# Performance work log

Hardware: AMD Instinct MI355X
Metric: run time of the kernel (lower is better)

## Reference

```python
import jax, jax.numpy as jnp
import numpy as np

# Photon library / detector geometry constants
NX, NY, NZ = 64, 64, 64          # voxel grid
N_VOX = NX * NY * NZ             # 262,144 voxels
N_PMT = 180                      # number of PMTs (columns of vis LUT)
N_CLUSTERS = 128                 # number of charge clusters (= len(dx))
PTS_PER_CLUSTER = 8192
TOTAL = N_CLUSTERS * PTS_PER_CLUSTER  # 1,048,576 charge points
LOWER = jnp.array([0.0, 0.0, 0.0], dtype=jnp.float32)
VOXEL_SIZE = jnp.array([1.0, 1.0, 1.0], dtype=jnp.float32)


def coord_to_voxel(coords):
    """Uniform-grid voxelization; x is the fastest-varying index so that
    vox_id + 1 is the neighbor voxel along x (matches the original backward)."""
    idx = jnp.floor((coords - LOWER) / VOXEL_SIZE).astype(jnp.int32)
    idx = jnp.clip(idx, 0, jnp.array([NX - 1, NY - 1, NZ - 1], dtype=jnp.int32))
    return idx[:, 0] + NX * (idx[:, 1] + NY * idx[:, 2])


def setup_inputs() -> dict:
    key = jax.random.key(0)
    k1, k2, k3, k4 = jax.random.split(key, 4)
    # coords: x in [8, 56) so dx in [-5, 5] stays in-grid; y,z in [0, 64)
    xyz = jax.random.uniform(
        k1, (TOTAL, 3),
        minval=jnp.array([8.0, 0.0, 0.0]),
        maxval=jnp.array([56.0, 64.0, 64.0]),
        dtype=jnp.float32,
    )
    q = jax.random.uniform(k2, (TOTAL, 1), dtype=jnp.float32)  # charge > 0
    batch = jnp.concatenate([xyz, q], axis=1)  # [TOTAL, 4]
    sizes = jnp.full((N_CLUSTERS,), PTS_PER_CLUSTER, dtype=jnp.int32)
    dx = jax.random.uniform(k3, (N_CLUSTERS,), minval=-3.0, maxval=3.0,
                            dtype=jnp.float32)
    dx_ranges = jnp.stack(
        [jnp.full((N_CLUSTERS,), -5.0, dtype=jnp.float32),
         jnp.full((N_CLUSTERS,), 5.0, dtype=jnp.float32)], axis=1)
    vis = jax.random.uniform(k4, (N_VOX, N_PMT), dtype=jnp.float32) * 1e-3
    return {"dx": dx, "batch": batch, "sizes": sizes,
            "dx_ranges": dx_ranges, "vis": vis}


def reference(dx, batch, sizes, dx_ranges, vis):
    # mask_dx(clamp=True): clamp per-cluster offsets to their ranges
    dx_c = jnp.clip(dx, dx_ranges[:, 0], dx_ranges[:, 1])  # [N_CLUSTERS]
    # cluster id per point (torch.repeat_interleave / torch.split equivalent)
    seg = jnp.repeat(jnp.arange(N_CLUSTERS, dtype=jnp.int32), sizes,
                     total_repeat_length=TOTAL)  # [TOTAL]
    coords = batch[:, :3].at[:, 0].add(dx_c[seg])  # shift x per cluster
    q = batch[:, 3]
    vox_ids = coord_to_voxel(coords)               # [TOTAL] int32
    vis_q = vis[vox_ids] * q[:, None]              # [TOTAL, N_PMT] gather+scale
    # ragged per-cluster sum (torch.split + per-segment sum, fused)
    pred = jax.ops.segment_sum(vis_q, seg, num_segments=N_CLUSTERS)
    return pred  # [N_CLUSTERS, N_PMT]
```

## Files before the change

### kernel.cpp

```cpp
#include <hip/hip_runtime.h>

#define N_PMT 180
#define N_PMT4 45
#define N_CLUSTERS 128
#define BPC 16
#define BLOCK 256
#define NWAVE (BLOCK / 64)


__global__ void prep_kernel(const float* __restrict__ dx,
                            const int* __restrict__ sizes,
                            const float* __restrict__ dx_ranges,
                            int* __restrict__ offsets,
                            float* __restrict__ dxc) {
    __shared__ int s[N_CLUSTERS];
    const int t = threadIdx.x;
    s[t] = sizes[t];
    float lo = dx_ranges[2 * t];
    float hi = dx_ranges[2 * t + 1];
    dxc[t] = fminf(fmaxf(dx[t], lo), hi);
    __syncthreads();
    int acc = 0;
    for (int i = 0; i < t; ++i) acc += s[i];
    offsets[t] = acc;
    if (t == N_CLUSTERS - 1) offsets[N_CLUSTERS] = acc + s[t];
}

__global__ __launch_bounds__(BLOCK) void gather_kernel(
    const float4* __restrict__ batch,
    const float4* __restrict__ vis4,
    const int*    __restrict__ offsets,
    const float*  __restrict__ dxc,
    float* __restrict__ out) {

    const int b     = blockIdx.x;
    const int c     = b / BPC;
    const int sub   = b % BPC;
    const int start = offsets[c];
    const int end   = offsets[c + 1];
    const int count = end - start;
    const int chunk = (count + BPC - 1) / BPC;
    const int s0 = start + sub * chunk;
    const int s1 = min(s0 + chunk, end);

    const int wave = threadIdx.x >> 6;
    const int lane = threadIdx.x & 63;

    const int wtotal = s1 - s0;
    const int per = (wtotal + NWAVE - 1) / NWAVE;
    const int ws0 = s0 + wave * per;
    const int ws1 = min(ws0 + per, s1);

    const float dxc_c = dxc[c];
    const bool active = (lane < N_PMT4);

    float4 accE = {0.f, 0.f, 0.f, 0.f};
    float4 accO = {0.f, 0.f, 0.f, 0.f};

    for (int base = ws0; base < ws1; base += 64) {
        const int p = base + lane;
        float q = 0.f;
        int vox = 0;
        if (p < ws1) {
            float4 pd = batch[p];
            float x = pd.x + dxc_c;
            int ix = (int)floorf(x);
            int iy = (int)floorf(pd.y);
            int iz = (int)floorf(pd.z);
            ix = max(0, min(63, ix));
            iy = max(0, min(63, iy));
            iz = max(0, min(63, iz));
            vox = ix + 64 * (iy + 64 * iz);
            q = pd.w;
        }
        #pragma unroll
        for (int j = 0; j < 64; j += 2) {
            const int   v0 = __builtin_amdgcn_readlane(vox, j);
            const float q0 = __uint_as_float(__builtin_amdgcn_readlane(__float_as_uint(q), j));
            const int   v1 = __builtin_amdgcn_readlane(vox, j + 1);
            const float q1 = __uint_as_float(__builtin_amdgcn_readlane(__float_as_uint(q), j + 1));
            if (active) {
                float4 r0 = vis4[(size_t)v0 * N_PMT4 + lane];
                float4 r1 = vis4[(size_t)v1 * N_PMT4 + lane];
                accE.x = fmaf(r0.x, q0, accE.x);
                accE.y = fmaf(r0.y, q0, accE.y);
                accE.z = fmaf(r0.z, q0, accE.z);
                accE.w = fmaf(r0.w, q0, accE.w);
                accO.x = fmaf(r1.x, q1, accO.x);
                accO.y = fmaf(r1.y, q1, accO.y);
                accO.z = fmaf(r1.z, q1, accO.z);
                accO.w = fmaf(r1.w, q1, accO.w);
            }
        }
    }

    __shared__ float sacc[N_PMT];
    for (int i = threadIdx.x; i < N_PMT; i += BLOCK) sacc[i] = 0.f;
    __syncthreads();
    if (active) {
        atomicAdd(&sacc[lane * 4 + 0], accE.x + accO.x);
        atomicAdd(&sacc[lane * 4 + 1], accE.y + accO.y);
        atomicAdd(&sacc[lane * 4 + 2], accE.z + accO.z);
        atomicAdd(&sacc[lane * 4 + 3], accE.w + accO.w);
    }
    __syncthreads();
    for (int i = threadIdx.x; i < N_PMT; i += BLOCK)
        atomicAdd(&out[c * N_PMT + i], sacc[i]);
}

extern "C" void kernel_launch(void* const* d_in, const int* in_sizes, int n_in,
                              void* d_out, int out_size, void* d_ws, size_t ws_size,
                              hipStream_t stream) {
    const float* dx        = (const float*)d_in[0];
    const float* batch     = (const float*)d_in[1];
    const int*   sizes     = (const int*)d_in[2];
    const float* dx_ranges = (const float*)d_in[3];
    const float* vis       = (const float*)d_in[4];
    float* out = (float*)d_out;

    int*   offsets = (int*)d_ws;
    float* dxc     = (float*)((char*)d_ws + sizeof(int) * (N_CLUSTERS + 1));

    hipMemsetAsync(out, 0, (size_t)out_size * sizeof(float), stream);

    prep_kernel<<<1, N_CLUSTERS, 0, stream>>>(dx, sizes, dx_ranges, offsets, dxc);

    gather_kernel<<<N_CLUSTERS * BPC, BLOCK, 0, stream>>>(
        (const float4*)batch, (const float4*)vis, offsets, dxc, out);
}
```

Baseline: 348.1 us.

## Bucket points by voxel and accumulate each vis row once per voxel

Replaces the per-point gather of vis rows with a counting sort: points are voxelized, counted per voxel, prefix-scanned and scattered into per-voxel buckets. Each vis row is then read once and applied to all of its points through shared-memory atomic accumulation into per-cluster accumulators, followed by a partial-buffer reduction. This cuts redundant random reads of the 188MB vis table, at the cost of several extra kernels, global atomics during counting and scatter, and heavy LDS atomic contention. The old gather path stays as a fallback when the workspace is too small.

```diff
diff --git a/kernel.cpp b/kernel.cpp
--- a/kernel.cpp
+++ b/kernel.cpp
@@ -1,17 +1,31 @@
 #include <hip/hip_runtime.h>
 
 #define N_PMT 180
-#define N_PMT4 45
 #define N_CLUSTERS 128
-#define BPC 16
-#define BLOCK 256
-#define NWAVE (BLOCK / 64)
-
+#define NVOX 262144
+#define VPB 1024
+#define K4_THREADS 1024
+#define K4_WAVES 16
+#define ACC_HALF 11520
+#define OUT_ELEMS (N_CLUSTERS * N_PMT)
+
+#define WS_OFFSC   0u
+#define WS_DXC     1024u
+#define WS_SCANNED 2048u
+#define WS_BSUM    1050624u
+#define WS_BBASE   1054720u
+#define WS_OFFS    1058816u
+#define WS_CURSOR  2107648u
+#define WS_VQ      3156224u
+#define WS_ENT     11544832u
+#define WS_PART    19933440u
+#define WS_NEED_ATOMIC 19933440ull
+#define WS_NEED_PART   43526400ull
 
 __global__ void prep_kernel(const float* __restrict__ dx,
                             const int* __restrict__ sizes,
                             const float* __restrict__ dx_ranges,
-                            int* __restrict__ offsets,
+                            int* __restrict__ offsC,
                             float* __restrict__ dxc) {
     __shared__ int s[N_CLUSTERS];
     const int t = threadIdx.x;
@@ -22,86 +36,204 @@
     __syncthreads();
     int acc = 0;
     for (int i = 0; i < t; ++i) acc += s[i];
-    offsets[t] = acc;
-    if (t == N_CLUSTERS - 1) offsets[N_CLUSTERS] = acc + s[t];
-}
-
+    offsC[t] = acc;
+    if (t == N_CLUSTERS - 1) offsC[N_CLUSTERS] = acc + s[t];
+}
+
+__global__ void k1_voxelize(const float4* __restrict__ batch,
+                            const int* __restrict__ offsC,
+                            const float* __restrict__ dxc,
+                            int n, uint2* __restrict__ vq,
+                            int* __restrict__ count) {
+    int i = blockIdx.x * 256 + threadIdx.x;
+    if (i >= n) return;
+    int lo = 0, hi = N_CLUSTERS - 1;
+    #pragma unroll
+    for (int s = 0; s < 7; ++s) {
+        int mid = (lo + hi + 1) >> 1;
+        if (i >= offsC[mid]) lo = mid; else hi = mid - 1;
+    }
+    const int c = lo;
+    float4 pd = batch[i];
+    float x = pd.x + dxc[c];
+    int ix = max(0, min(63, (int)floorf(x)));
+    int iy = max(0, min(63, (int)floorf(pd.y)));
+    int iz = max(0, min(63, (int)floorf(pd.z)));
+    int vox = ix + 64 * (iy + 64 * iz);
+    vq[i] = make_uint2((unsigned)vox | ((unsigned)c << 18), __float_as_uint(pd.w));
+    atomicAdd(&count[vox], 1);
+}
+
+__global__ void k2a_scan(const int* __restrict__ count,
+                         int* __restrict__ scanned,
+                         int* __restrict__ bsum) {
+    __shared__ int s[256];
+    const int b = blockIdx.x, t = threadIdx.x, i = b * 256 + t;
+    int x = count[i];
+    s[t] = x; __syncthreads();
+    for (int d = 1; d < 256; d <<= 1) {
+        int v_ = (t >= d) ? s[t - d] : 0; __syncthreads();
+        s[t] += v_; __syncthreads();
+    }
+    scanned[i] = s[t] - x;
+    if (t == 255) bsum[b] = s[255];
+}
+
+__global__ void k2b_scan(const int* __restrict__ bsum, int* __restrict__ bbase) {
+    __shared__ int s[1024];
+    const int t = threadIdx.x;
+    int x = bsum[t];
+    s[t] = x; __syncthreads();
+    for (int d = 1; d < 1024; d <<= 1) {
+        int v_ = (t >= d) ? s[t - d] : 0; __syncthreads();
+        s[t] += v_; __syncthreads();
+    }
+    bbase[t] = s[t] - x;
+}
+
+__global__ void k2c_fix(const int* __restrict__ scanned,
+                        const int* __restrict__ bbase,
+                        int* __restrict__ offs,
+                        int* __restrict__ cursor, int total) {
+    const int b = blockIdx.x, t = threadIdx.x, i = b * 256 + t;
+    int o = scanned[i] + bbase[b];
+    offs[i] = o;
+    cursor[i] = o;
+    if (i == NVOX - 1) offs[NVOX] = total;
+}
+
+__global__ void k3_scatter(const uint2* __restrict__ vq,
+                           int* __restrict__ cursor,
+                           uint2* __restrict__ entries, int n) {
+    int i = blockIdx.x * 256 + threadIdx.x;
+    if (i >= n) return;
+    uint2 e = vq[i];
+    int vox = (int)(e.x & 0x3FFFFu);
+    unsigned c = e.x >> 18;
+    int pos = atomicAdd(&cursor[vox], 1);
+    entries[pos] = make_uint2(e.y, c);
+}
+
+__global__ __launch_bounds__(K4_THREADS) void k4_accum(
+    const float* __restrict__ vis,
+    const int* __restrict__ offs,
+    const uint2* __restrict__ entries,
+    float* __restrict__ out,
+    float* __restrict__ partial, int mode) {
+
+    __shared__ float acc[ACC_HALF];
+    const int h  = blockIdx.x & 1;
+    const int vb = blockIdx.x >> 1;
+    for (int j = threadIdx.x; j < ACC_HALF; j += K4_THREADS) acc[j] = 0.f;
+    __syncthreads();
+
+    const int wv = threadIdx.x >> 6;
+    const int l  = threadIdx.x & 63;
+    const bool lB = (l < 26);
+    const int v0 = vb * VPB + wv * (VPB / K4_WAVES);
+    const int v1 = v0 + (VPB / K4_WAVES);
+    const int hoff = h * 90;
+
+    for (int v = v0; v < v1; ++v) {
+        int e0 = offs[v], e1 = offs[v + 1];
+        if (e0 >= e1) continue;
+        const float* rowp = vis + (size_t)v * N_PMT + hoff;
+        float rA = rowp[l];
+        float rB = lB ? rowp[64 + l] : 0.f;
+        for (int e = e0; e < e1; ++e) {
+            uint2 ent = entries[e];
+            float q = __uint_as_float(ent.x);
+            int   c = (int)ent.y;
+            float* ab = &acc[c * 90];
+            atomicAdd(&ab[l], rA * q);
+            if (lB) atomicAdd(&ab[64 + l], rB * q);
+        }
+    }
+    __syncthreads();
+
+    if (mode == 0) {
+        float* dst = partial + (size_t)blockIdx.x * ACC_HALF;
+        for (int j = threadIdx.x; j < ACC_HALF; j += K4_THREADS) dst[j] = acc[j];
+    } else {
+        for (int j = threadIdx.x; j < ACC_HALF; j += K4_THREADS) {
+            int c = j / 90, pp = j - c * 90;
+            atomicAdd(&out[c * N_PMT + hoff + pp], acc[j]);
+        }
+    }
+}
+
+__global__ void k5_reduce(const float* __restrict__ partial, float* __restrict__ out) {
+    const int ob = blockIdx.x % 90;
+    const int vb = blockIdx.x / 90;
+    const int o = ob * 256 + threadIdx.x;
+    const int c = o / N_PMT, p = o - c * N_PMT;
+    const int h = p / 90, pp = p - h * 90;
+    float s = 0.f;
+    const int base = vb * 32;
+    #pragma unroll 8
+    for (int k = 0; k < 32; ++k) {
+        int vc = base + k;
+        s += partial[(size_t)(vc * 2 + h) * ACC_HALF + c * 90 + pp];
+    }
+    atomicAdd(&out[o], s);
+}
+
+#define BPC 16
+#define BLOCK 256
+#define NWAVE (BLOCK / 64)
 __global__ __launch_bounds__(BLOCK) void gather_kernel(
     const float4* __restrict__ batch,
     const float4* __restrict__ vis4,
     const int*    __restrict__ offsets,
     const float*  __restrict__ dxc,
     float* __restrict__ out) {
-
-    const int b     = blockIdx.x;
-    const int c     = b / BPC;
-    const int sub   = b % BPC;
-    const int start = offsets[c];
-    const int end   = offsets[c + 1];
+    const int b = blockIdx.x;
+    const int c = b / BPC, sub = b % BPC;
+    const int start = offsets[c], end = offsets[c + 1];
     const int count = end - start;
     const int chunk = (count + BPC - 1) / BPC;
     const int s0 = start + sub * chunk;
     const int s1 = min(s0 + chunk, end);
-
-    const int wave = threadIdx.x >> 6;
-    const int lane = threadIdx.x & 63;
-
+    const int wave = threadIdx.x >> 6, lane = threadIdx.x & 63;
     const int wtotal = s1 - s0;
     const int per = (wtotal + NWAVE - 1) / NWAVE;
     const int ws0 = s0 + wave * per;
     const int ws1 = min(ws0 + per, s1);
-
     const float dxc_c = dxc[c];
-    const bool active = (lane < N_PMT4);
-
+    const bool active = (lane < 45);
     float4 accE = {0.f, 0.f, 0.f, 0.f};
-    float4 accO = {0.f, 0.f, 0.f, 0.f};
-
     for (int base = ws0; base < ws1; base += 64) {
         const int p = base + lane;
-        float q = 0.f;
-        int vox = 0;
+        float q = 0.f; int vox = 0;
         if (p < ws1) {
             float4 pd = batch[p];
-            float x = pd.x + dxc_c;
-            int ix = (int)floorf(x);
-            int iy = (int)floorf(pd.y);
-            int iz = (int)floorf(pd.z);
-            ix = max(0, min(63, ix));
-            iy = max(0, min(63, iy));
-            iz = max(0, min(63, iz));
+            int ix = max(0, min(63, (int)floorf(pd.x + dxc_c)));
+            int iy = max(0, min(63, (int)floorf(pd.y)));
+            int iz = max(0, min(63, (int)floorf(pd.z)));
             vox = ix + 64 * (iy + 64 * iz);
             q = pd.w;
         }
         #pragma unroll
-        for (int j = 0; j < 64; j += 2) {
-            const int   v0 = __builtin_amdgcn_readlane(vox, j);
-            const float q0 = __uint_as_float(__builtin_amdgcn_readlane(__float_as_uint(q), j));
-            const int   v1 = __builtin_amdgcn_readlane(vox, j + 1);
-            const float q1 = __uint_as_float(__builtin_amdgcn_readlane(__float_as_uint(q), j + 1));
+        for (int j = 0; j < 64; ++j) {
+            const int   v  = __builtin_amdgcn_readlane(vox, j);
+            const float qj = __uint_as_float(__builtin_amdgcn_readlane(__float_as_uint(q), j));
             if (active) {
-                float4 r0 = vis4[(size_t)v0 * N_PMT4 + lane];
-                float4 r1 = vis4[(size_t)v1 * N_PMT4 + lane];
-                accE.x = fmaf(r0.x, q0, accE.x);
-                accE.y = fmaf(r0.y, q0, accE.y);
-                accE.z = fmaf(r0.z, q0, accE.z);
-                accE.w = fmaf(r0.w, q0, accE.w);
-                accO.x = fmaf(r1.x, q1, accO.x);
-                accO.y = fmaf(r1.y, q1, accO.y);
-                accO.z = fmaf(r1.z, q1, accO.z);
-                accO.w = fmaf(r1.w, q1, accO.w);
+                float4 r = vis4[(size_t)v * 45 + lane];
+                accE.x = fmaf(r.x, qj, accE.x);
+                accE.y = fmaf(r.y, qj, accE.y);
+                accE.z = fmaf(r.z, qj, accE.z);
+                accE.w = fmaf(r.w, qj, accE.w);
             }
         }
     }
-
     __shared__ float sacc[N_PMT];
     for (int i = threadIdx.x; i < N_PMT; i += BLOCK) sacc[i] = 0.f;
     __syncthreads();
     if (active) {
-        atomicAdd(&sacc[lane * 4 + 0], accE.x + accO.x);
-        atomicAdd(&sacc[lane * 4 + 1], accE.y + accO.y);
-        atomicAdd(&sacc[lane * 4 + 2], accE.z + accO.z);
-        atomicAdd(&sacc[lane * 4 + 3], accE.w + accO.w);
+        atomicAdd(&sacc[lane * 4 + 0], accE.x);
+        atomicAdd(&sacc[lane * 4 + 1], accE.y);
+        atomicAdd(&sacc[lane * 4 + 2], accE.z);
+        atomicAdd(&sacc[lane * 4 + 3], accE.w);
     }
     __syncthreads();
     for (int i = threadIdx.x; i < N_PMT; i += BLOCK)
@@ -117,14 +249,38 @@
     const float* dx_ranges = (const float*)d_in[3];
     const float* vis       = (const float*)d_in[4];
     float* out = (float*)d_out;
-
-    int*   offsets = (int*)d_ws;
-    float* dxc     = (float*)((char*)d_ws + sizeof(int) * (N_CLUSTERS + 1));
+    char*  wsb = (char*)d_ws;
+    const int n = in_sizes[1] / 4;
+
+    int*   offsC   = (int*)(wsb + WS_OFFSC);
+    float* dxc     = (float*)(wsb + WS_DXC);
+    int*   scanned = (int*)(wsb + WS_SCANNED);
+    int*   bsum    = (int*)(wsb + WS_BSUM);
+    int*   bbase   = (int*)(wsb + WS_BBASE);
+    int*   offs    = (int*)(wsb + WS_OFFS);
+    int*   cursor  = (int*)(wsb + WS_CURSOR);
+    uint2* vq      = (uint2*)(wsb + WS_VQ);
+    uint2* entries = (uint2*)(wsb + WS_ENT);
+    float* part    = (float*)(wsb + WS_PART);
 
     hipMemsetAsync(out, 0, (size_t)out_size * sizeof(float), stream);
-
-    prep_kernel<<<1, N_CLUSTERS, 0, stream>>>(dx, sizes, dx_ranges, offsets, dxc);
-
-    gather_kernel<<<N_CLUSTERS * BPC, BLOCK, 0, stream>>>(
-        (const float4*)batch, (const float4*)vis, offsets, dxc, out);
-}
+    prep_kernel<<<1, N_CLUSTERS, 0, stream>>>(dx, sizes, dx_ranges, offsC, dxc);
+
+    if (ws_size >= WS_NEED_ATOMIC) {
+        const int mode = (ws_size >= WS_NEED_PART) ? 0 : 1;
+        hipMemsetAsync(cursor, 0, NVOX * sizeof(int), stream);
+        k1_voxelize<<<(n + 255) / 256, 256, 0, stream>>>(
+            (const float4*)batch, offsC, dxc, n, vq, cursor);
+        k2a_scan<<<NVOX / 256, 256, 0, stream>>>(cursor, scanned, bsum);
+        k2b_scan<<<1, 1024, 0, stream>>>(bsum, bbase);
+        k2c_fix<<<NVOX / 256, 256, 0, stream>>>(scanned, bbase, offs, cursor, n);
+        k3_scatter<<<(n + 255) / 256, 256, 0, stream>>>(vq, cursor, entries, n);
+        k4_accum<<<(NVOX / VPB) * 2, K4_THREADS, 0, stream>>>(
+            vis, offs, entries, out, part, mode);
+        if (mode == 0)
+            k5_reduce<<<720, 256, 0, stream>>>(part, out);
+    } else {
+        gather_kernel<<<N_CLUSTERS * BPC, BLOCK, 0, stream>>>(
+            (const float4*)batch, (const float4*)vis, offsC, dxc, out);
+    }
+}
```

Result: slower. 1.302 ms (+274.2%).
